# Optimization experiments

Measured on AMD Instinct MI355X. Metric: run time of the kernel, lower is better.

Reference implementation:

```python
import jax, jax.numpy as jnp
import numpy as np

N_NODES = 50000
K_EIG = 512
F_DIM = 128


def setup_inputs() -> dict:
    key = jax.random.key(0)
    k1, k2, k3 = jax.random.split(key, 3)
    eigenvectors = jax.random.normal(k1, (N_NODES, K_EIG), dtype=jnp.float32)
    spectral_filters = jax.random.normal(k2, (K_EIG,), dtype=jnp.float32)
    x = jax.random.normal(k3, (N_NODES, F_DIM), dtype=jnp.float32)
    return {"eigenvectors": eigenvectors, "spectral_filters": spectral_filters, "x": x}


def reference(eigenvectors, spectral_filters, x):
    # U @ diag(g) @ U.T @ x  ==  U @ (g[:, None] * (U.T @ x)); relu epilogue.
    spec = eigenvectors.T @ x                      # [k, f]
    logits = eigenvectors @ (spectral_filters[:, None] * spec)  # [n, f]
    return jax.nn.relu(logits)
```

## Files before the change

### kernel.cpp

```cpp
#include <hip/hip_runtime.h>
#include <hip/hip_bf16.h>

#define N_NODES 50000
#define K_EIG   512
#define F_DIM   128
#define NPAD    51200
#define NSPLITS 200
#define CHUNK   256
#define NT32    1600

typedef __attribute__((ext_vector_type(8))) short bf16x8;
typedef __attribute__((ext_vector_type(4))) short s16x4;
typedef __attribute__((ext_vector_type(4))) float f32x4;
typedef __attribute__((ext_vector_type(2))) unsigned u32x2;

static __device__ __forceinline__ unsigned pk2(float lo, float hi) {
    unsigned short a = __builtin_bit_cast(unsigned short, __float2bfloat16(lo));
    unsigned short b = __builtin_bit_cast(unsigned short, __float2bfloat16(hi));
    return ((unsigned)b << 16) | (unsigned)a;
}

static __device__ __forceinline__ short f2bf(float f) {
    union { float f; unsigned u; } v; v.f = f;
    unsigned r = v.u + 0x7fffu + ((v.u >> 16) & 1u);
    return (short)(r >> 16);
}

static __device__ __forceinline__ float bf2f(unsigned short u) {
    union { unsigned u; float f; } v; v.u = ((unsigned)u) << 16;
    return v.f;
}

__global__ __launch_bounds__(256) void prep_x(const float* __restrict__ x,
                                              unsigned short* __restrict__ xTa)
{
    const int n0 = blockIdx.x * 64;
    const int f0 = blockIdx.y * 64;
    const int fa = threadIdx.x & 15;
    const int nb = threadIdx.x >> 4;
    const int n  = n0 + 4 * nb;
    const int f  = f0 + 4 * fa;

    float r[4][4];
    #pragma unroll
    for (int jj = 0; jj < 4; ++jj) {
        int nr = n + jj;
        if (nr < N_NODES) {
            f32x4 v = *reinterpret_cast<const f32x4*>(x + (long)nr * F_DIM + f);
            r[jj][0] = v[0]; r[jj][1] = v[1]; r[jj][2] = v[2]; r[jj][3] = v[3];
        } else {
            r[jj][0] = r[jj][1] = r[jj][2] = r[jj][3] = 0.f;
        }
    }
    const int nt32 = n >> 5;
    const int hpart = ((n >> 3) & 3) * 16;
    const int slot  = 4 * (nb & 1);
    #pragma unroll
    for (int i = 0; i < 4; ++i) {
        int fi = f + i;
        size_t ad = ((size_t)((fi >> 4) * NT32 + nt32) * 64 + hpart + (fi & 15)) * 8 + slot;
        u32x2 w; w[0] = pk2(r[0][i], r[1][i]); w[1] = pk2(r[2][i], r[3][i]);
        *reinterpret_cast<u32x2*>(xTa + ad) = w;
    }
}

__global__ __launch_bounds__(256) void k_spec_f(
    const float* __restrict__ U, const unsigned short* __restrict__ xTa,
    unsigned short* __restrict__ part2)
{
    __shared__ unsigned char lds1[2][64 * 128];

    const int split = blockIdx.x;
    const int kt    = blockIdx.y;
    const int tid   = threadIdx.x;
    const int wid   = tid >> 6;
    const int lane  = tid & 63;
    const int h     = lane >> 4;
    const int m     = lane & 15;
    const int k0    = kt * 64;
    const int nbeg  = split * CHUNK;

    const int kq = tid & 15;
    const int nq = tid >> 4;

    f32x4 acc[4][2];
    #pragma unroll
    for (int s = 0; s < 4; ++s)
        #pragma unroll
        for (int t = 0; t < 2; ++t)
            #pragma unroll
            for (int e = 0; e < 4; ++e) acc[s][t][e] = 0.f;

    const unsigned short* Bl = xTa + (size_t)lane * 8;
    const int ftb = wid * 2;

    float  r[4][4];
    bf16x8 bfr[2][2];

    #pragma unroll
    for (int j = 0; j < 4; ++j) {
        int n = nbeg + 4 * nq + j;
        if (n < N_NODES) {
            f32x4 v = *reinterpret_cast<const f32x4*>(U + (long)n * K_EIG + k0 + 4 * kq);
            r[j][0] = v[0]; r[j][1] = v[1]; r[j][2] = v[2]; r[j][3] = v[3];
        } else {
            r[j][0] = r[j][1] = r[j][2] = r[j][3] = 0.f;
        }
    }
    #pragma unroll
    for (int sub = 0; sub < 2; ++sub)
        #pragma unroll
        for (int t = 0; t < 2; ++t)
            bfr[sub][t] = *reinterpret_cast<const bf16x8*>(
                Bl + (size_t)((ftb + t) * NT32 + (nbeg >> 5) + sub) * 512);

    #pragma unroll
    for (int step = 0; step < 4; ++step) {
        const int ntile = nbeg + 64 * step;
        const int buf   = step & 1;

        float  rN[4][4];
        bf16x8 bN[2][2];
        if (step < 3) {
            const int nt2 = ntile + 64;
            #pragma unroll
            for (int j = 0; j < 4; ++j) {
                int n = nt2 + 4 * nq + j;
                if (n < N_NODES) {
                    f32x4 v = *reinterpret_cast<const f32x4*>(
                        U + (long)n * K_EIG + k0 + 4 * kq);
                    rN[j][0] = v[0]; rN[j][1] = v[1]; rN[j][2] = v[2]; rN[j][3] = v[3];
                } else {
                    rN[j][0] = rN[j][1] = rN[j][2] = rN[j][3] = 0.f;
                }
            }
            #pragma unroll
            for (int sub = 0; sub < 2; ++sub)
                #pragma unroll
                for (int t = 0; t < 2; ++t)
                    bN[sub][t] = *reinterpret_cast<const bf16x8*>(
                        Bl + (size_t)((ftb + t) * NT32 + (nt2 >> 5) + sub) * 512);
        }

        #pragma unroll
        for (int i = 0; i < 4; ++i) {
            int kl = 4 * kq + i;
            unsigned lo = pk2(r[0][i], r[1][i]);
            unsigned hi = pk2(r[2][i], r[3][i]);
            int byte = (kl * 128 + 8 * nq) ^ ((kl & 7) << 4);
            *reinterpret_cast<unsigned long long*>(&lds1[buf][byte]) =
                ((unsigned long long)hi << 32) | (unsigned long long)lo;
        }
        __syncthreads();

        #pragma unroll
        for (int sub = 0; sub < 2; ++sub) {
            bf16x8 af[4];
            #pragma unroll
            for (int s = 0; s < 4; ++s) {
                int row  = 16 * s + m;
                int byte = (row * 128 + 64 * sub + 16 * h) ^ ((m & 7) << 4);
                af[s] = *reinterpret_cast<const bf16x8*>(&lds1[buf][byte]);
            }
            #pragma unroll
            for (int s = 0; s < 4; ++s)
                #pragma unroll
                for (int t = 0; t < 2; ++t)
                    acc[s][t] = __builtin_amdgcn_mfma_f32_16x16x32_bf16(
                        af[s], bfr[sub][t], acc[s][t], 0, 0, 0);
        }

        if (step < 3) {
            #pragma unroll
            for (int j = 0; j < 4; ++j)
                #pragma unroll
                for (int i = 0; i < 4; ++i) r[j][i] = rN[j][i];
            #pragma unroll
            for (int sub = 0; sub < 2; ++sub)
                #pragma unroll
                for (int t = 0; t < 2; ++t) bfr[sub][t] = bN[sub][t];
        }
    }

    unsigned short* pb = part2 + (((size_t)(kt * NSPLITS + split)) * 256 + tid) * 32;
    #pragma unroll
    for (int s = 0; s < 4; ++s) {
        bf16x8 v;
        #pragma unroll
        for (int e = 0; e < 4; ++e) {
            v[e]     = f2bf(acc[s][0][e]);
            v[e + 4] = f2bf(acc[s][1][e]);
        }
        *reinterpret_cast<bf16x8*>(pb + s * 8) = v;
    }
}

__global__ __launch_bounds__(256) void k_reduce1(
    const unsigned short* __restrict__ part2, float* __restrict__ part3)
{
    const int q  = blockIdx.x * 256 + threadIdx.x;
    const int pg = blockIdx.y;
    const int kt = q >> 11;
    const int tp = (q >> 3) & 255;
    const int sl = q & 7;
    f32x4 s; s[0] = s[1] = s[2] = s[3] = 0.f;
    const int pend = pg * 25 + 25;
    for (int p = pg * 25; p < pend; ++p) {
        s16x4 v = *reinterpret_cast<const s16x4*>(
            part2 + (((size_t)(kt * NSPLITS + p)) * 256 + tp) * 32 + sl * 4);
        s[0] += bf2f((unsigned short)v[0]); s[1] += bf2f((unsigned short)v[1]);
        s[2] += bf2f((unsigned short)v[2]); s[3] += bf2f((unsigned short)v[3]);
    }
    *reinterpret_cast<f32x4*>(part3 + ((size_t)pg * 16384 + q) * 4) = s;
}

__global__ __launch_bounds__(256) void k_reduce2(
    const float* __restrict__ part3, const float* __restrict__ g,
    unsigned short* __restrict__ specbfa)
{
    const int q = blockIdx.x * 256 + threadIdx.x;
    f32x4 s; s[0] = s[1] = s[2] = s[3] = 0.f;
    #pragma unroll
    for (int pg = 0; pg < 8; ++pg) {
        f32x4 v = *reinterpret_cast<const f32x4*>(part3 + ((size_t)pg * 16384 + q) * 4);
        s[0] += v[0]; s[1] += v[1]; s[2] += v[2]; s[3] += v[3];
    }
    const int kt = q >> 11, tp = (q >> 3) & 255, sl = q & 7;
    const int wid = tp >> 6, le = tp & 63, hh = le >> 4, mm = le & 15;
    const int ss = sl >> 1, tt = sl & 1;
    const int f = wid * 32 + tt * 16 + mm;
    const int k = kt * 64 + ss * 16 + hh * 4;
    f32x4 gv = *reinterpret_cast<const f32x4*>(g + k);
    s16x4 o;
    #pragma unroll
    for (int e = 0; e < 4; ++e) o[e] = f2bf(s[e] * gv[e]);
    const int lanep = ((k >> 3) & 3) * 16 + (f & 15);
    size_t ad = ((size_t)((f >> 4) * 16 + (k >> 5)) * 64 + lanep) * 8 + (k & 7);
    *reinterpret_cast<s16x4*>(specbfa + ad) = o;
}

__global__ __launch_bounds__(256) void k_out_f32(
    const float* __restrict__ U, const unsigned short* __restrict__ specbfa,
    float* __restrict__ out)
{
    const int tid  = threadIdx.x;
    const int wid  = tid >> 6;
    const int lane = tid & 63;
    const int h = lane >> 4, m = lane & 15;
    const int wr = wid >> 1, wc = wid & 1;
    const int nbase = blockIdx.x * 64 + wr * 32;
    const int fbase = wc * 64;

    const float* Arow[2];
    #pragma unroll
    for (int i = 0; i < 2; ++i) {
        int n  = nbase + 16 * i + m;
        int nc = (n < N_NODES) ? n : (N_NODES - 1);
        Arow[i] = U + (size_t)nc * K_EIG + 8 * h;
    }
    const unsigned short* Blp[4];
    #pragma unroll
    for (int t = 0; t < 4; ++t)
        Blp[t] = specbfa + ((size_t)(4 * wc + t) * 8192 + lane * 8);

    f32x4 acc[2][4];
    #pragma unroll
    for (int i = 0; i < 2; ++i)
        #pragma unroll
        for (int t = 0; t < 4; ++t)
            #pragma unroll
            for (int e = 0; e < 4; ++e) acc[i][t][e] = 0.f;

    f32x4 loC[2], hiC[2]; bf16x8 bC[4];
    #pragma unroll
    for (int i = 0; i < 2; ++i) {
        loC[i] = *reinterpret_cast<const f32x4*>(Arow[i]);
        hiC[i] = *reinterpret_cast<const f32x4*>(Arow[i] + 4);
    }
    #pragma unroll
    for (int t = 0; t < 4; ++t)
        bC[t] = *reinterpret_cast<const bf16x8*>(Blp[t]);

    for (int kb = 0; kb < 16; ++kb) {
        int kn = (kb + 1 < 16) ? kb + 1 : 0;
        f32x4 loN[2], hiN[2]; bf16x8 bN[4];
        #pragma unroll
        for (int i = 0; i < 2; ++i) {
            loN[i] = *reinterpret_cast<const f32x4*>(Arow[i] + kn * 32);
            hiN[i] = *reinterpret_cast<const f32x4*>(Arow[i] + kn * 32 + 4);
        }
        #pragma unroll
        for (int t = 0; t < 4; ++t)
            bN[t] = *reinterpret_cast<const bf16x8*>(Blp[t] + (size_t)kn * 512);

        bf16x8 a[2];
        #pragma unroll
        for (int i = 0; i < 2; ++i)
            #pragma unroll
            for (int j = 0; j < 4; ++j) {
                a[i][j]     = f2bf(loC[i][j]);
                a[i][j + 4] = f2bf(hiC[i][j]);
            }
        #pragma unroll
        for (int i = 0; i < 2; ++i)
            #pragma unroll
            for (int t = 0; t < 4; ++t)
                acc[i][t] = __builtin_amdgcn_mfma_f32_16x16x32_bf16(
                    a[i], bC[t], acc[i][t], 0, 0, 0);

        #pragma unroll
        for (int i = 0; i < 2; ++i) { loC[i] = loN[i]; hiC[i] = hiN[i]; }
        #pragma unroll
        for (int t = 0; t < 4; ++t) bC[t] = bN[t];
    }

    #pragma unroll
    for (int i = 0; i < 2; ++i)
        #pragma unroll
        for (int r = 0; r < 4; ++r) {
            int nn = nbase + 16 * i + 4 * h + r;
            if (nn < N_NODES) {
                float* orow = out + (long)nn * F_DIM + fbase + m;
                #pragma unroll
                for (int t = 0; t < 4; ++t)
                    orow[16 * t] = fmaxf(acc[i][t][r], 0.f);
            }
        }
}

__global__ __launch_bounds__(256) void k_spec_v1(
    const float* __restrict__ U, const float* __restrict__ g,
    const float* __restrict__ x, float* __restrict__ specT)
{
    const int kt    = blockIdx.x;
    const int split = blockIdx.y;
    const int tid   = threadIdx.x;
    const int wid   = tid >> 6;
    const int lane  = tid & 63;
    const int h     = lane >> 4;
    const int m     = lane & 15;
    const int k0 = kt * 64;
    const int f0 = wid * 32;
    const int chunk1 = 782;
    const int n_start = split * chunk1;
    int n_end = n_start + chunk1;
    if (n_end > N_NODES) n_end = N_NODES;

    f32x4 acc[4][2];
    #pragma unroll
    for (int s = 0; s < 4; ++s)
        #pragma unroll
        for (int t = 0; t < 2; ++t)
            #pragma unroll
            for (int e = 0; e < 4; ++e) acc[s][t][e] = 0.f;

    for (int nb = n_start; nb < n_end; nb += 32) {
        bf16x8 a[4]; bf16x8 b[2];
        const int nrow = nb + 8 * h;
        #pragma unroll
        for (int j = 0; j < 8; ++j) {
            int nn = nrow + j;
            bool valid = (nn < n_end);
            int nc = valid ? nn : (n_end - 1);
            const float* Urow = U + (long)nc * K_EIG + k0 + m;
            const float* Xrow = x + (long)nc * F_DIM + f0 + m;
            #pragma unroll
            for (int s = 0; s < 4; ++s) {
                short bv = f2bf(Urow[16 * s]);
                a[s][j] = valid ? bv : (short)0;
            }
            #pragma unroll
            for (int t = 0; t < 2; ++t) {
                short bv = f2bf(Xrow[16 * t]);
                b[t][j] = valid ? bv : (short)0;
            }
        }
        #pragma unroll
        for (int s = 0; s < 4; ++s)
            #pragma unroll
            for (int t = 0; t < 2; ++t)
                acc[s][t] = __builtin_amdgcn_mfma_f32_16x16x32_bf16(
                    a[s], b[t], acc[s][t], 0, 0, 0);
    }
    #pragma unroll
    for (int s = 0; s < 4; ++s)
        #pragma unroll
        for (int t = 0; t < 2; ++t)
            #pragma unroll
            for (int r = 0; r < 4; ++r) {
                int k = k0 + 16 * s + 4 * h + r;
                int f = f0 + 16 * t + m;
                atomicAdd(&specT[(long)f * K_EIG + k], acc[s][t][r] * g[k]);
            }
}

__global__ __launch_bounds__(256) void k_out_v1(
    const float* __restrict__ U, const float* __restrict__ specT,
    float* __restrict__ out)
{
    const int tid  = threadIdx.x;
    const int wid  = tid >> 6;
    const int lane = tid & 63;
    const int h = lane >> 4, m = lane & 15;
    const int wr = wid >> 1, wc = wid & 1;
    const int nbase = blockIdx.x * 128 + wr * 64;
    const int fbase = wc * 64;

    f32x4 acc[4][4];
    #pragma unroll
    for (int i = 0; i < 4; ++i)
        #pragma unroll
        for (int t = 0; t < 4; ++t)
            #pragma unroll
            for (int e = 0; e < 4; ++e) acc[i][t][e] = 0.f;

    for (int kb = 0; kb < K_EIG; kb += 32) {
        bf16x8 a[4], b[4];
        #pragma unroll
        for (int i = 0; i < 4; ++i) {
            int nn = nbase + 16 * i + m;
            bool valid = (nn < N_NODES);
            int nc = valid ? nn : (N_NODES - 1);
            const f32x4* p = reinterpret_cast<const f32x4*>(
                U + (long)nc * K_EIG + kb + 8 * h);
            f32x4 lo = p[0], hi = p[1];
            #pragma unroll
            for (int j = 0; j < 4; ++j) {
                short b0 = f2bf(lo[j]), b1 = f2bf(hi[j]);
                a[i][j]     = valid ? b0 : (short)0;
                a[i][j + 4] = valid ? b1 : (short)0;
            }
        }
        #pragma unroll
        for (int t = 0; t < 4; ++t) {
            const f32x4* p = reinterpret_cast<const f32x4*>(
                specT + (long)(fbase + 16 * t + m) * K_EIG + kb + 8 * h);
            f32x4 lo = p[0], hi = p[1];
            #pragma unroll
            for (int j = 0; j < 4; ++j) {
                b[t][j]     = f2bf(lo[j]);
                b[t][j + 4] = f2bf(hi[j]);
            }
        }
        #pragma unroll
        for (int i = 0; i < 4; ++i)
            #pragma unroll
            for (int t = 0; t < 4; ++t)
                acc[i][t] = __builtin_amdgcn_mfma_f32_16x16x32_bf16(
                    a[i], b[t], acc[i][t], 0, 0, 0);
    }
    #pragma unroll
    for (int i = 0; i < 4; ++i)
        #pragma unroll
        for (int r = 0; r < 4; ++r) {
            int nn = nbase + 16 * i + 4 * h + r;
            if (nn < N_NODES) {
                float* orow = out + (long)nn * F_DIM + fbase + m;
                #pragma unroll
                for (int t = 0; t < 4; ++t)
                    orow[16 * t] = fmaxf(acc[i][t][r], 0.f);
            }
        }
}

extern "C" void kernel_launch(void* const* d_in, const int* in_sizes, int n_in,
                              void* d_out, int out_size, void* d_ws, size_t ws_size,
                              hipStream_t stream) {
    const float* U = (const float*)d_in[0];
    const float* g = (const float*)d_in[1];
    const float* x = (const float*)d_in[2];
    float* out = (float*)d_out;

    const size_t OFF_XTA   = 0;
    const size_t OFF_PART2 = 13107200;
    const size_t OFF_PART3 = 39321600;
    const size_t OFF_SPECA = 41418752;
    const size_t WS_NEEDED = 41549824;

    if (ws_size >= WS_NEEDED) {
        unsigned short* xTa     = (unsigned short*)((char*)d_ws + OFF_XTA);
        unsigned short* part2   = (unsigned short*)((char*)d_ws + OFF_PART2);
        float*          part3   = (float*)((char*)d_ws + OFF_PART3);
        unsigned short* specbfa = (unsigned short*)((char*)d_ws + OFF_SPECA);

        dim3 gx(NPAD / 64, F_DIM / 64);
        prep_x<<<gx, 256, 0, stream>>>(x, xTa);

        dim3 g1(NSPLITS, K_EIG / 64);
        k_spec_f<<<g1, 256, 0, stream>>>(U, xTa, part2);

        dim3 gr1(64, 8);
        k_reduce1<<<gr1, 256, 0, stream>>>(part2, part3);
        k_reduce2<<<64, 256, 0, stream>>>(part3, g, specbfa);

        int nb2 = (N_NODES + 63) / 64;
        k_out_f32<<<nb2, 256, 0, stream>>>(U, specbfa, out);
    } else {
        float* specT = (float*)d_ws;
        hipMemsetAsync(specT, 0, (size_t)K_EIG * F_DIM * sizeof(float), stream);
        dim3 g1(K_EIG / 64, 64);
        k_spec_v1<<<g1, 256, 0, stream>>>(U, g, x, specT);
        int nb2 = (N_NODES + 127) / 128;
        k_out_v1<<<nb2, 256, 0, stream>>>(U, specT, out);
    }
}
```

Measured before the change: 96.86 us.

## Split spectral GEMM blocks into independent single-wave blocks without barriers

Each 256-thread block of the U^T·x kernel becomes four 64-thread blocks, indexed by blockIdx.z, that each handle one feature tile pair. Each wave now loads and converts the full 64×64 U tile into its own LDS double buffer, with no __syncthreads. This removes block-wide barriers and gives finer-grained scheduling, at the cost of four times the U global loads and conversion work per tile. It relies on L2 to absorb the redundant reads.

```diff
diff --git a/kernel.cpp b/kernel.cpp
--- a/kernel.cpp
+++ b/kernel.cpp
@@ -64,7 +64,7 @@
     }
 }
 
-__global__ __launch_bounds__(256) void k_spec_f(
+__global__ __launch_bounds__(64) void k_spec_w(
     const float* __restrict__ U, const unsigned short* __restrict__ xTa,
     unsigned short* __restrict__ part2)
 {
@@ -72,16 +72,13 @@
 
     const int split = blockIdx.x;
     const int kt    = blockIdx.y;
-    const int tid   = threadIdx.x;
-    const int wid   = tid >> 6;
-    const int lane  = tid & 63;
-    const int h     = lane >> 4;
-    const int m     = lane & 15;
-    const int k0    = kt * 64;
-    const int nbeg  = split * CHUNK;
-
-    const int kq = tid & 15;
-    const int nq = tid >> 4;
+    const int wid   = blockIdx.z;
+    const int lane  = threadIdx.x;
+    const int h = lane >> 4, m = lane & 15;
+    const int k0   = kt * 64;
+    const int nbeg = split * CHUNK;
+    const int kq = lane & 15;
+    const int nq = lane >> 4;
 
     f32x4 acc[4][2];
     #pragma unroll
@@ -94,64 +91,71 @@
     const unsigned short* Bl = xTa + (size_t)lane * 8;
     const int ftb = wid * 2;
 
-    float  r[4][4];
-    bf16x8 bfr[2][2];
-
-    #pragma unroll
-    for (int j = 0; j < 4; ++j) {
-        int n = nbeg + 4 * nq + j;
-        if (n < N_NODES) {
-            f32x4 v = *reinterpret_cast<const f32x4*>(U + (long)n * K_EIG + k0 + 4 * kq);
-            r[j][0] = v[0]; r[j][1] = v[1]; r[j][2] = v[2]; r[j][3] = v[3];
-        } else {
-            r[j][0] = r[j][1] = r[j][2] = r[j][3] = 0.f;
+    f32x4  r[4][4];
+    bf16x8 bc[2][2], bn[2][2];
+
+    #pragma unroll
+    for (int q = 0; q < 4; ++q) {
+        const int nqq = nq + 4 * q;
+        #pragma unroll
+        for (int j = 0; j < 4; ++j) {
+            int n = nbeg + 4 * nqq + j;
+            if (n < N_NODES)
+                r[q][j] = *reinterpret_cast<const f32x4*>(
+                    U + (size_t)n * K_EIG + k0 + 4 * kq);
+            else {
+                r[q][j][0] = r[q][j][1] = r[q][j][2] = r[q][j][3] = 0.f;
+            }
         }
     }
     #pragma unroll
     for (int sub = 0; sub < 2; ++sub)
         #pragma unroll
         for (int t = 0; t < 2; ++t)
-            bfr[sub][t] = *reinterpret_cast<const bf16x8*>(
+            bc[sub][t] = *reinterpret_cast<const bf16x8*>(
                 Bl + (size_t)((ftb + t) * NT32 + (nbeg >> 5) + sub) * 512);
 
     #pragma unroll
-    for (int step = 0; step < 4; ++step) {
-        const int ntile = nbeg + 64 * step;
-        const int buf   = step & 1;
-
-        float  rN[4][4];
-        bf16x8 bN[2][2];
-        if (step < 3) {
-            const int nt2 = ntile + 64;
-            #pragma unroll
-            for (int j = 0; j < 4; ++j) {
-                int n = nt2 + 4 * nq + j;
-                if (n < N_NODES) {
-                    f32x4 v = *reinterpret_cast<const f32x4*>(
-                        U + (long)n * K_EIG + k0 + 4 * kq);
-                    rN[j][0] = v[0]; rN[j][1] = v[1]; rN[j][2] = v[2]; rN[j][3] = v[3];
-                } else {
-                    rN[j][0] = rN[j][1] = rN[j][2] = rN[j][3] = 0.f;
-                }
-            }
-            #pragma unroll
-            for (int sub = 0; sub < 2; ++sub)
-                #pragma unroll
-                for (int t = 0; t < 2; ++t)
-                    bN[sub][t] = *reinterpret_cast<const bf16x8*>(
-                        Bl + (size_t)((ftb + t) * NT32 + (nt2 >> 5) + sub) * 512);
-        }
-
+    for (int q = 0; q < 4; ++q) {
+        const int nqq = nq + 4 * q;
         #pragma unroll
         for (int i = 0; i < 4; ++i) {
             int kl = 4 * kq + i;
-            unsigned lo = pk2(r[0][i], r[1][i]);
-            unsigned hi = pk2(r[2][i], r[3][i]);
-            int byte = (kl * 128 + 8 * nq) ^ ((kl & 7) << 4);
-            *reinterpret_cast<unsigned long long*>(&lds1[buf][byte]) =
+            unsigned lo = pk2(r[q][0][i], r[q][1][i]);
+            unsigned hi = pk2(r[q][2][i], r[q][3][i]);
+            int byte = (kl * 128 + 8 * nqq) ^ ((kl & 7) << 4);
+            *reinterpret_cast<unsigned long long*>(&lds1[0][byte]) =
                 ((unsigned long long)hi << 32) | (unsigned long long)lo;
         }
-        __syncthreads();
+    }
+
+    #pragma unroll
+    for (int tile = 0; tile < 4; ++tile) {
+        const int buf = tile & 1;
+
+        if (tile < 3) {
+            const int nb2 = nbeg + 64 * (tile + 1);
+            #pragma unroll
+            for (int q = 0; q < 4; ++q) {
+                const int nqq = nq + 4 * q;
+                #pragma unroll
+                for (int j = 0; j < 4; ++j) {
+                    int n = nb2 + 4 * nqq + j;
+                    if (n < N_NODES)
+                        r[q][j] = *reinterpret_cast<const f32x4*>(
+                            U + (size_t)n * K_EIG + k0 + 4 * kq);
+                    else {
+                        r[q][j][0] = r[q][j][1] = r[q][j][2] = r[q][j][3] = 0.f;
+                    }
+                }
+            }
+            #pragma unroll
+            for (int sub = 0; sub < 2; ++sub)
+                #pragma unroll
+                for (int t = 0; t < 2; ++t)
+                    bn[sub][t] = *reinterpret_cast<const bf16x8*>(
+                        Bl + (size_t)((ftb + t) * NT32 + (nb2 >> 5) + sub) * 512);
+        }
 
         #pragma unroll
         for (int sub = 0; sub < 2; ++sub) {
@@ -167,22 +171,32 @@
                 #pragma unroll
                 for (int t = 0; t < 2; ++t)
                     acc[s][t] = __builtin_amdgcn_mfma_f32_16x16x32_bf16(
-                        af[s], bfr[sub][t], acc[s][t], 0, 0, 0);
-        }
-
-        if (step < 3) {
-            #pragma unroll
-            for (int j = 0; j < 4; ++j)
-                #pragma unroll
-                for (int i = 0; i < 4; ++i) r[j][i] = rN[j][i];
+                        af[s], bc[sub][t], acc[s][t], 0, 0, 0);
+        }
+
+        if (tile < 3) {
+            #pragma unroll
+            for (int q = 0; q < 4; ++q) {
+                const int nqq = nq + 4 * q;
+                #pragma unroll
+                for (int i = 0; i < 4; ++i) {
+                    int kl = 4 * kq + i;
+                    unsigned lo = pk2(r[q][0][i], r[q][1][i]);
+                    unsigned hi = pk2(r[q][2][i], r[q][3][i]);
+                    int byte = (kl * 128 + 8 * nqq) ^ ((kl & 7) << 4);
+                    *reinterpret_cast<unsigned long long*>(&lds1[buf ^ 1][byte]) =
+                        ((unsigned long long)hi << 32) | (unsigned long long)lo;
+                }
+            }
             #pragma unroll
             for (int sub = 0; sub < 2; ++sub)
                 #pragma unroll
-                for (int t = 0; t < 2; ++t) bfr[sub][t] = bN[sub][t];
-        }
-    }
-
-    unsigned short* pb = part2 + (((size_t)(kt * NSPLITS + split)) * 256 + tid) * 32;
+                for (int t = 0; t < 2; ++t) bc[sub][t] = bn[sub][t];
+        }
+    }
+
+    unsigned short* pb = part2 +
+        (((size_t)(kt * NSPLITS + split)) * 256 + (wid * 64 + lane)) * 32;
     #pragma unroll
     for (int s = 0; s < 4; ++s) {
         bf16x8 v;
@@ -486,8 +500,8 @@
         dim3 gx(NPAD / 64, F_DIM / 64);
         prep_x<<<gx, 256, 0, stream>>>(x, xTa);
 
-        dim3 g1(NSPLITS, K_EIG / 64);
-        k_spec_f<<<g1, 256, 0, stream>>>(U, xTa, part2);
+        dim3 g1(NSPLITS, K_EIG / 64, 4);
+        k_spec_w<<<g1, 64, 0, stream>>>(U, xTa, part2);
 
         dim3 gr1(64, 8);
         k_reduce1<<<gr1, 256, 0, stream>>>(part2, part3);
```

After: 123.3 us. +27.3%, slower.
